# Optimization experiments

Measured on AMD Instinct MI355X. Metric: run time of the kernel, lower is better.

Reference implementation:

```python
import jax, jax.numpy as jnp
import numpy as np

N_NODES = 100000
N_EDGES = 2000000
D = 128
REL_TYPES = 64


def setup_inputs() -> dict:
    key = jax.random.key(0)
    k1, k2, k3, k4 = jax.random.split(key, 4)
    z = jax.random.normal(k1, (N_NODES, D), dtype=jnp.float32)
    edge_index = jax.random.randint(k2, (2, N_EDGES), 0, N_NODES, dtype=jnp.int64)
    rel_id = jax.random.randint(k3, (N_EDGES,), 0, REL_TYPES, dtype=jnp.int64)
    rel = jax.random.normal(k4, (REL_TYPES, D), dtype=jnp.float32)
    return {"z": z, "edge_index": edge_index, "rel_id": rel_id, "rel": rel}


def reference(z, edge_index, rel_id, rel):
    # DistMult: sigmoid(sum_d z[src,d] * rel[rel_id,d] * z[dst,d])
    src = z[edge_index[0]]          # [E, D]
    dst = z[edge_index[1]]          # [E, D]
    r = rel[rel_id]                 # [E, D]
    scores = jnp.sum(src * r * dst, axis=1)  # [E]
    return jax.nn.sigmoid(scores)
```

## Files before the change

kernel.cpp:

```cpp
#include <hip/hip_runtime.h>
#include <hip/hip_fp16.h>
#include <stdint.h>


#define NSRC 8
#define NDST 64
#define NBKT 512
#define CNT_STRIDE 16
#define SC_BLOCKS 512

__global__ __launch_bounds__(256) void convert_kernel(
    const float* __restrict__ x, __half* __restrict__ xh, int n8)
{
    const int i = blockIdx.x * blockDim.x + threadIdx.x;
    if (i >= n8) return;
    const float4 f0 = ((const float4*)x)[2 * i];
    const float4 f1 = ((const float4*)x)[2 * i + 1];
    union { __half2 h2[4]; uint4 u; } o;
    o.h2[0] = __floats2half2_rn(f0.x, f0.y);
    o.h2[1] = __floats2half2_rn(f0.z, f0.w);
    o.h2[2] = __floats2half2_rn(f1.x, f1.y);
    o.h2[3] = __floats2half2_rn(f1.z, f1.w);
    ((uint4*)xh)[i] = o.u;
}

__device__ __forceinline__ uint32_t bucket_of2(uint32_t s, uint32_t d, uint32_t nn) {
    uint32_t ss = (s * (uint32_t)NSRC) / nn; if (ss > NSRC - 1) ss = NSRC - 1;
    uint32_t ds = (d * (uint32_t)NDST) / nn; if (ds > NDST - 1) ds = NDST - 1;
    return ss * NDST + ds;
}

__global__ __launch_bounds__(256) void scatter_agg_kernel(
    const int* __restrict__ src, const int* __restrict__ dst,
    const int* __restrict__ relid, int E, int nn, int cap,
    uint32_t* __restrict__ counters, uint64_t* __restrict__ binned)
{
    __shared__ uint32_t hist[NBKT];
    __shared__ uint32_t cursor[NBKT];

    const int chunk = (E + (int)gridDim.x - 1) / (int)gridDim.x;
    const int lo = blockIdx.x * chunk;
    const int hi = (lo + chunk < E) ? lo + chunk : E;

    for (int t = threadIdx.x; t < NBKT; t += 256) hist[t] = 0;
    __syncthreads();

    for (int i = lo + (int)threadIdx.x; i < hi; i += 256) {
        const uint32_t b = bucket_of2((uint32_t)src[i], (uint32_t)dst[i], (uint32_t)nn);
        atomicAdd(&hist[b], 1u);
    }
    __syncthreads();

    for (int t = threadIdx.x; t < NBKT; t += 256) {
        const uint32_t c = hist[t];
        cursor[t] = c ? atomicAdd(&counters[t * CNT_STRIDE], c) : 0u;
    }
    __syncthreads();

    for (int i = lo + (int)threadIdx.x; i < hi; i += 256) {
        const uint32_t s = (uint32_t)src[i];
        const uint32_t d = (uint32_t)dst[i];
        const uint32_t r = (uint32_t)relid[i];
        const uint32_t b = bucket_of2(s, d, (uint32_t)nn);
        const uint32_t pos = atomicAdd(&cursor[b], 1u);
        if (pos < (uint32_t)cap)
            binned[(size_t)b * (size_t)cap + pos] =
                (uint64_t)s | ((uint64_t)d << 17) | ((uint64_t)r << 34) | ((uint64_t)i << 40);
    }
}

__global__ __launch_bounds__(256) void distmult_bucketed_kernel(
    const __half* __restrict__ zh,
    const uint64_t* __restrict__ binned,
    const uint32_t* __restrict__ counters,
    const __half* __restrict__ relh,
    float* __restrict__ out,
    int cap, int cpb)
{
    const int k     = blockIdx.x & 7;
    const int t     = blockIdx.x >> 3;
    const int j     = t / cpb;
    const int chunk = t - j * cpb;
    const int bkt   = k * NDST + j;

    uint32_t cnt = counters[bkt * CNT_STRIDE];
    if (cnt > (uint32_t)cap) cnt = (uint32_t)cap;
    const uint32_t el_blk = (uint32_t)chunk * 32u;
    if (el_blk >= cnt) return;

    __shared__ uint4 rel_lds[1024];
    {
        const uint4* rsrc = (const uint4*)relh;
        #pragma unroll
        for (int q = 0; q < 4; q++)
            rel_lds[threadIdx.x + 256 * q] = rsrc[threadIdx.x + 256 * q];
    }
    __syncthreads();

    const int g    = threadIdx.x >> 4;
    const int lane = threadIdx.x & 15;
    const uint32_t el0 = el_blk + (uint32_t)g * 2u;
    if (el0 >= cnt) return;
    const bool has1 = (el0 + 1u < cnt);

    const uint64_t* bb = binned + (size_t)bkt * (size_t)cap;
    const uint64_t p0 = bb[el0];
    const uint64_t p1 = has1 ? bb[el0 + 1u] : p0;

    const uint32_t s0 = (uint32_t)p0 & 0x1FFFFu;
    const uint32_t d0 = (uint32_t)(p0 >> 17) & 0x1FFFFu;
    const uint32_t r0 = (uint32_t)(p0 >> 34) & 0x3Fu;
    const uint32_t e0 = (uint32_t)(p0 >> 40);
    const uint32_t s1 = (uint32_t)p1 & 0x1FFFFu;
    const uint32_t d1 = (uint32_t)(p1 >> 17) & 0x1FFFFu;
    const uint32_t r1 = (uint32_t)(p1 >> 34) & 0x3Fu;
    const uint32_t e1 = (uint32_t)(p1 >> 40);

    union { uint4 u; __half2 h2[4]; } A0, B0, A1, B1, R0, R1;
    A0.u = ((const uint4*)(zh + (size_t)s0 * 128))[lane];
    B0.u = ((const uint4*)(zh + (size_t)d0 * 128))[lane];
    A1.u = ((const uint4*)(zh + (size_t)s1 * 128))[lane];
    B1.u = ((const uint4*)(zh + (size_t)d1 * 128))[lane];
    R0.u = rel_lds[r0 * 16 + lane];
    R1.u = rel_lds[r1 * 16 + lane];

    float v0 = 0.f, v1 = 0.f;
    #pragma unroll
    for (int q = 0; q < 4; q++) {
        const float2 a0 = __half22float2(A0.h2[q]);
        const float2 b0 = __half22float2(B0.h2[q]);
        const float2 c0 = __half22float2(R0.h2[q]);
        v0 += a0.x * c0.x * b0.x + a0.y * c0.y * b0.y;
        const float2 a1 = __half22float2(A1.h2[q]);
        const float2 b1 = __half22float2(B1.h2[q]);
        const float2 c1 = __half22float2(R1.h2[q]);
        v1 += a1.x * c1.x * b1.x + a1.y * c1.y * b1.y;
    }

    #pragma unroll
    for (int off = 8; off > 0; off >>= 1) {
        v0 += __shfl_down(v0, off, 16);
        v1 += __shfl_down(v1, off, 16);
    }

    if (lane == 0) {
        out[e0] = 1.0f / (1.0f + __expf(-v0));
        if (has1) out[e1] = 1.0f / (1.0f + __expf(-v1));
    }
}

__global__ __launch_bounds__(256) void distmult_f16_lds_kernel(
    const __half* __restrict__ zh,
    const int* __restrict__ src_idx, const int* __restrict__ dst_idx,
    const int* __restrict__ rel_id, const __half* __restrict__ relh,
    float* __restrict__ out, int E)
{
    __shared__ uint4 rel_lds[1024];
    {
        const uint4* rsrc = (const uint4*)relh;
        #pragma unroll
        for (int q = 0; q < 4; q++)
            rel_lds[threadIdx.x + 256 * q] = rsrc[threadIdx.x + 256 * q];
    }
    __syncthreads();

    const int gtid = blockIdx.x * blockDim.x + threadIdx.x;
    const int g = gtid >> 4;
    const int lane = threadIdx.x & 15;
    const int e0 = g * 2, e1 = e0 + 1;
    if (e0 >= E) return;
    const bool has1 = (e1 < E);

    const int s0 = src_idx[e0], d0 = dst_idx[e0], r0 = rel_id[e0];
    const int s1 = has1 ? src_idx[e1] : s0;
    const int d1 = has1 ? dst_idx[e1] : d0;
    const int r1 = has1 ? rel_id[e1]  : r0;

    union { uint4 u; __half2 h2[4]; } A0, B0, A1, B1, R0, R1;
    A0.u = ((const uint4*)(zh + (size_t)s0 * 128))[lane];
    B0.u = ((const uint4*)(zh + (size_t)d0 * 128))[lane];
    A1.u = ((const uint4*)(zh + (size_t)s1 * 128))[lane];
    B1.u = ((const uint4*)(zh + (size_t)d1 * 128))[lane];
    R0.u = rel_lds[r0 * 16 + lane];
    R1.u = rel_lds[r1 * 16 + lane];

    float v0 = 0.f, v1 = 0.f;
    #pragma unroll
    for (int q = 0; q < 4; q++) {
        const float2 a0 = __half22float2(A0.h2[q]);
        const float2 b0 = __half22float2(B0.h2[q]);
        const float2 c0 = __half22float2(R0.h2[q]);
        v0 += a0.x * c0.x * b0.x + a0.y * c0.y * b0.y;
        const float2 a1 = __half22float2(A1.h2[q]);
        const float2 b1 = __half22float2(B1.h2[q]);
        const float2 c1 = __half22float2(R1.h2[q]);
        v1 += a1.x * c1.x * b1.x + a1.y * c1.y * b1.y;
    }
    #pragma unroll
    for (int off = 8; off > 0; off >>= 1) {
        v0 += __shfl_down(v0, off, 16);
        v1 += __shfl_down(v1, off, 16);
    }
    if (lane == 0) {
        const float o0 = 1.0f / (1.0f + __expf(-v0));
        if (has1) {
            const float o1 = 1.0f / (1.0f + __expf(-v1));
            *((float2*)(out + e0)) = make_float2(o0, o1);
        } else {
            out[e0] = o0;
        }
    }
}

__global__ __launch_bounds__(256) void distmult_f32_kernel(
    const float* __restrict__ z,
    const int* __restrict__ src_idx, const int* __restrict__ dst_idx,
    const int* __restrict__ rel_id, const float* __restrict__ rel,
    float* __restrict__ out, int E)
{
    const int gtid = blockIdx.x * blockDim.x + threadIdx.x;
    const int e = gtid >> 4;
    const int lane = threadIdx.x & 15;
    if (e >= E) return;
    const int s = src_idx[e], d = dst_idx[e], r = rel_id[e];
    const float4* zs = (const float4*)(z + (size_t)s * 128);
    const float4* zd = (const float4*)(z + (size_t)d * 128);
    const float4* rr = (const float4*)(rel + (size_t)r * 128);
    const float4 a0 = zs[lane], a1 = zs[lane + 16];
    const float4 b0 = zd[lane], b1 = zd[lane + 16];
    const float4 c0 = rr[lane], c1 = rr[lane + 16];
    float v = a0.x * c0.x * b0.x + a0.y * c0.y * b0.y
            + a0.z * c0.z * b0.z + a0.w * c0.w * b0.w
            + a1.x * c1.x * b1.x + a1.y * c1.y * b1.y
            + a1.z * c1.z * b1.z + a1.w * c1.w * b1.w;
    #pragma unroll
    for (int off = 8; off > 0; off >>= 1) v += __shfl_down(v, off, 16);
    if (lane == 0) out[e] = 1.0f / (1.0f + __expf(-v));
}

extern "C" void kernel_launch(void* const* d_in, const int* in_sizes, int n_in,
                              void* d_out, int out_size, void* d_ws, size_t ws_size,
                              hipStream_t stream) {
    const float* z     = (const float*)d_in[0];
    const int*   eidx  = (const int*)d_in[1];
    const int*   relid = (const int*)d_in[2];
    const float* rel   = (const float*)d_in[3];
    float*       out   = (float*)d_out;

    const int nz   = in_sizes[0];
    const int E    = in_sizes[2];
    const int nrel = in_sizes[3];
    const int nn   = nz / 128;
    const int* src = eidx;
    const int* dst = eidx + E;

    const int mean_b = E / NBKT;
    int cap = mean_b + E / 8192 + 512;
    cap = (cap + 31) & ~31;
    const int cpb = cap / 32;

    const size_t sz_zh    = (size_t)nz * sizeof(__half);
    const size_t off_rh   = (sz_zh + 255) & ~(size_t)255;
    const size_t sz_rh    = (size_t)nrel * sizeof(__half);
    const size_t off_cnt  = (off_rh + sz_rh + 255) & ~(size_t)255;
    const size_t sz_cnt   = (size_t)NBKT * CNT_STRIDE * 4;
    const size_t off_bin  = (off_cnt + sz_cnt + 255) & ~(size_t)255;
    const size_t sz_bin   = (size_t)NBKT * (size_t)cap * 8;
    const size_t need     = off_bin + sz_bin;

    const bool rel_ok  = (nrel == 64 * 128);
    const bool bits_ok = (nn <= 131072) && (E <= (1 << 21)) && (nz % 8 == 0);

    if (ws_size >= need && rel_ok && bits_ok) {
        char* ws = (char*)d_ws;
        __half*   zh       = (__half*)(ws);
        __half*   rh       = (__half*)(ws + off_rh);
        uint32_t* counters = (uint32_t*)(ws + off_cnt);
        uint64_t* binned   = (uint64_t*)(ws + off_bin);

        const int n8z = nz / 8, n8r = nrel / 8;
        convert_kernel<<<(n8z + 255) / 256, 256, 0, stream>>>(z, zh, n8z);
        convert_kernel<<<(n8r + 255) / 256, 256, 0, stream>>>(rel, rh, n8r);
        hipMemsetAsync(counters, 0, sz_cnt, stream);
        scatter_agg_kernel<<<SC_BLOCKS, 256, 0, stream>>>(
            src, dst, relid, E, nn, cap, counters, binned);
        distmult_bucketed_kernel<<<NSRC * NDST * cpb, 256, 0, stream>>>(
            zh, binned, counters, rh, out, cap, cpb);
    } else if (ws_size >= off_rh + sz_rh && rel_ok && nz % 8 == 0) {
        __half* zh = (__half*)d_ws;
        __half* rh = (__half*)((char*)d_ws + off_rh);
        const int n8z = nz / 8, n8r = nrel / 8;
        convert_kernel<<<(n8z + 255) / 256, 256, 0, stream>>>(z, zh, n8z);
        convert_kernel<<<(n8r + 255) / 256, 256, 0, stream>>>(rel, rh, n8r);
        const int groups = (E + 1) / 2;
        const int blocks = (groups * 16 + 255) / 256;
        distmult_f16_lds_kernel<<<blocks, 256, 0, stream>>>(
            zh, src, dst, relid, rh, out, E);
    } else {
        const int blocks = (E * 16 + 255) / 256;
        distmult_f32_kernel<<<blocks, 256, 0, stream>>>(z, src, dst, relid, rel, out, E);
    }
}
```

Baseline: 265.1 us.

## Cache scatter payloads in registers, use 8-lane groups with fdot2

The scatter kernel now reads src, dst and rel_id once. It keeps each edge's packed payload and bucket in registers between the histogram pass and the write pass, where before it re-read the index arrays a second time. The bucketed scoring kernel now gives each edge to 8 lanes instead of two edges per 16 lanes. Each lane loads two 16-byte chunks, and the products are computed with packed half multiplies feeding the fdot2 builtin, which cuts conversion work and the shuffle depth. The risks are higher register pressure in scatter (16 payloads per thread), the chunk size now setting the grid size, and fp16 multiplication of a*r before accumulation, which lowers precision.

Result: faster. 231.2 us (-12.8%).

```diff
diff --git a/kernel.cpp b/kernel.cpp
--- a/kernel.cpp
+++ b/kernel.cpp
@@ -8,6 +8,35 @@
 #define NBKT 512
 #define CNT_STRIDE 16
 #define SC_BLOCKS 512
+#define PE 16
+
+#if defined(__has_builtin)
+#if __has_builtin(__builtin_amdgcn_fdot2)
+#define HAS_FDOT2 1
+#endif
+#endif
+
+typedef _Float16 hv2 __attribute__((ext_vector_type(2)));
+
+__device__ __forceinline__ float dot3_accum(uint32_t a, uint32_t r, uint32_t b,
+                                            float acc)
+{
+#ifdef HAS_FDOT2
+    union { uint32_t u; hv2 v; } A, R, B;
+    A.u = a; R.u = r; B.u = b;
+    const hv2 t = A.v * R.v;
+    return __builtin_amdgcn_fdot2(t, B.v, acc, false);
+#else
+    union { uint32_t u; __half2 h; } A, R, B;
+    A.u = a; R.u = r; B.u = b;
+    const float2 af = __half22float2(A.h);
+    const float2 rf = __half22float2(R.h);
+    const float2 bf = __half22float2(B.h);
+    acc = fmaf(af.x * rf.x, bf.x, acc);
+    acc = fmaf(af.y * rf.y, bf.y, acc);
+    return acc;
+#endif
+}
 
 __global__ __launch_bounds__(256) void convert_kernel(
     const float* __restrict__ x, __half* __restrict__ xh, int n8)
@@ -30,7 +59,7 @@
     return ss * NDST + ds;
 }
 
-__global__ __launch_bounds__(256) void scatter_agg_kernel(
+__global__ __launch_bounds__(256) void scatter_reg_kernel(
     const int* __restrict__ src, const int* __restrict__ dst,
     const int* __restrict__ relid, int E, int nn, int cap,
     uint32_t* __restrict__ counters, uint64_t* __restrict__ binned)
@@ -45,9 +74,24 @@
     for (int t = threadIdx.x; t < NBKT; t += 256) hist[t] = 0;
     __syncthreads();
 
-    for (int i = lo + (int)threadIdx.x; i < hi; i += 256) {
-        const uint32_t b = bucket_of2((uint32_t)src[i], (uint32_t)dst[i], (uint32_t)nn);
-        atomicAdd(&hist[b], 1u);
+    uint64_t pay[PE];
+    uint32_t bkt[PE];
+
+    #pragma unroll
+    for (int p = 0; p < PE; p++) {
+        const int i = lo + p * 256 + (int)threadIdx.x;
+        if (i < hi) {
+            const uint32_t s = (uint32_t)src[i];
+            const uint32_t d = (uint32_t)dst[i];
+            const uint32_t r = (uint32_t)relid[i];
+            const uint32_t b = bucket_of2(s, d, (uint32_t)nn);
+            pay[p] = (uint64_t)s | ((uint64_t)d << 17)
+                   | ((uint64_t)r << 34) | ((uint64_t)i << 40);
+            bkt[p] = b;
+            atomicAdd(&hist[b], 1u);
+        } else {
+            bkt[p] = 0xFFFFFFFFu;
+        }
     }
     __syncthreads();
 
@@ -57,19 +101,17 @@
     }
     __syncthreads();
 
-    for (int i = lo + (int)threadIdx.x; i < hi; i += 256) {
-        const uint32_t s = (uint32_t)src[i];
-        const uint32_t d = (uint32_t)dst[i];
-        const uint32_t r = (uint32_t)relid[i];
-        const uint32_t b = bucket_of2(s, d, (uint32_t)nn);
-        const uint32_t pos = atomicAdd(&cursor[b], 1u);
-        if (pos < (uint32_t)cap)
-            binned[(size_t)b * (size_t)cap + pos] =
-                (uint64_t)s | ((uint64_t)d << 17) | ((uint64_t)r << 34) | ((uint64_t)i << 40);
-    }
-}
-
-__global__ __launch_bounds__(256) void distmult_bucketed_kernel(
+    #pragma unroll
+    for (int p = 0; p < PE; p++) {
+        if (bkt[p] != 0xFFFFFFFFu) {
+            const uint32_t pos = atomicAdd(&cursor[bkt[p]], 1u);
+            if (pos < (uint32_t)cap)
+                binned[(size_t)bkt[p] * (size_t)cap + pos] = pay[p];
+        }
+    }
+}
+
+__global__ __launch_bounds__(256) void distmult_bucketed8_kernel(
     const __half* __restrict__ zh,
     const uint64_t* __restrict__ binned,
     const uint32_t* __restrict__ counters,
@@ -97,56 +139,41 @@
     }
     __syncthreads();
 
-    const int g    = threadIdx.x >> 4;
-    const int lane = threadIdx.x & 15;
-    const uint32_t el0 = el_blk + (uint32_t)g * 2u;
-    if (el0 >= cnt) return;
-    const bool has1 = (el0 + 1u < cnt);
-
-    const uint64_t* bb = binned + (size_t)bkt * (size_t)cap;
-    const uint64_t p0 = bb[el0];
-    const uint64_t p1 = has1 ? bb[el0 + 1u] : p0;
-
-    const uint32_t s0 = (uint32_t)p0 & 0x1FFFFu;
-    const uint32_t d0 = (uint32_t)(p0 >> 17) & 0x1FFFFu;
-    const uint32_t r0 = (uint32_t)(p0 >> 34) & 0x3Fu;
-    const uint32_t e0 = (uint32_t)(p0 >> 40);
-    const uint32_t s1 = (uint32_t)p1 & 0x1FFFFu;
-    const uint32_t d1 = (uint32_t)(p1 >> 17) & 0x1FFFFu;
-    const uint32_t r1 = (uint32_t)(p1 >> 34) & 0x3Fu;
-    const uint32_t e1 = (uint32_t)(p1 >> 40);
-
-    union { uint4 u; __half2 h2[4]; } A0, B0, A1, B1, R0, R1;
-    A0.u = ((const uint4*)(zh + (size_t)s0 * 128))[lane];
-    B0.u = ((const uint4*)(zh + (size_t)d0 * 128))[lane];
-    A1.u = ((const uint4*)(zh + (size_t)s1 * 128))[lane];
-    B1.u = ((const uint4*)(zh + (size_t)d1 * 128))[lane];
-    R0.u = rel_lds[r0 * 16 + lane];
-    R1.u = rel_lds[r1 * 16 + lane];
-
-    float v0 = 0.f, v1 = 0.f;
+    const int g    = threadIdx.x >> 3;
+    const int lane = threadIdx.x & 7;
+    const uint32_t el = el_blk + (uint32_t)g;
+    if (el >= cnt) return;
+
+    const uint64_t p = binned[(size_t)bkt * (size_t)cap + el];
+    const uint32_t s   = (uint32_t)p & 0x1FFFFu;
+    const uint32_t d   = (uint32_t)(p >> 17) & 0x1FFFFu;
+    const uint32_t r   = (uint32_t)(p >> 34) & 0x3Fu;
+    const uint32_t eid = (uint32_t)(p >> 40);
+
+    union U4 { uint4 q; uint32_t w[4]; };
+    const uint4* sb = (const uint4*)(zh + (size_t)s * 128);
+    const uint4* db = (const uint4*)(zh + (size_t)d * 128);
+    U4 A0, A1, B0, B1, R0, R1;
+    A0.q = sb[lane * 2];
+    A1.q = sb[lane * 2 + 1];
+    B0.q = db[lane * 2];
+    B1.q = db[lane * 2 + 1];
+    R0.q = rel_lds[r * 16 + lane * 2];
+    R1.q = rel_lds[r * 16 + lane * 2 + 1];
+
+    float acc = 0.f;
     #pragma unroll
     for (int q = 0; q < 4; q++) {
-        const float2 a0 = __half22float2(A0.h2[q]);
-        const float2 b0 = __half22float2(B0.h2[q]);
-        const float2 c0 = __half22float2(R0.h2[q]);
-        v0 += a0.x * c0.x * b0.x + a0.y * c0.y * b0.y;
-        const float2 a1 = __half22float2(A1.h2[q]);
-        const float2 b1 = __half22float2(B1.h2[q]);
-        const float2 c1 = __half22float2(R1.h2[q]);
-        v1 += a1.x * c1.x * b1.x + a1.y * c1.y * b1.y;
-    }
-
-    #pragma unroll
-    for (int off = 8; off > 0; off >>= 1) {
-        v0 += __shfl_down(v0, off, 16);
-        v1 += __shfl_down(v1, off, 16);
-    }
-
-    if (lane == 0) {
-        out[e0] = 1.0f / (1.0f + __expf(-v0));
-        if (has1) out[e1] = 1.0f / (1.0f + __expf(-v1));
-    }
+        acc = dot3_accum(A0.w[q], R0.w[q], B0.w[q], acc);
+        acc = dot3_accum(A1.w[q], R1.w[q], B1.w[q], acc);
+    }
+
+    #pragma unroll
+    for (int off = 4; off > 0; off >>= 1)
+        acc += __shfl_down(acc, off, 8);
+
+    if (lane == 0)
+        out[eid] = 1.0f / (1.0f + __expf(-acc));
 }
 
 __global__ __launch_bounds__(256) void distmult_f16_lds_kernel(
@@ -176,25 +203,20 @@
     const int d1 = has1 ? dst_idx[e1] : d0;
     const int r1 = has1 ? rel_id[e1]  : r0;
 
-    union { uint4 u; __half2 h2[4]; } A0, B0, A1, B1, R0, R1;
-    A0.u = ((const uint4*)(zh + (size_t)s0 * 128))[lane];
-    B0.u = ((const uint4*)(zh + (size_t)d0 * 128))[lane];
-    A1.u = ((const uint4*)(zh + (size_t)s1 * 128))[lane];
-    B1.u = ((const uint4*)(zh + (size_t)d1 * 128))[lane];
-    R0.u = rel_lds[r0 * 16 + lane];
-    R1.u = rel_lds[r1 * 16 + lane];
+    union U4 { uint4 q; uint32_t w[4]; };
+    U4 A0, B0, A1, B1, R0, R1;
+    A0.q = ((const uint4*)(zh + (size_t)s0 * 128))[lane];
+    B0.q = ((const uint4*)(zh + (size_t)d0 * 128))[lane];
+    A1.q = ((const uint4*)(zh + (size_t)s1 * 128))[lane];
+    B1.q = ((const uint4*)(zh + (size_t)d1 * 128))[lane];
+    R0.q = rel_lds[r0 * 16 + lane];
+    R1.q = rel_lds[r1 * 16 + lane];
 
     float v0 = 0.f, v1 = 0.f;
     #pragma unroll
     for (int q = 0; q < 4; q++) {
-        const float2 a0 = __half22float2(A0.h2[q]);
-        const float2 b0 = __half22float2(B0.h2[q]);
-        const float2 c0 = __half22float2(R0.h2[q]);
-        v0 += a0.x * c0.x * b0.x + a0.y * c0.y * b0.y;
-        const float2 a1 = __half22float2(A1.h2[q]);
-        const float2 b1 = __half22float2(B1.h2[q]);
-        const float2 c1 = __half22float2(R1.h2[q]);
-        v1 += a1.x * c1.x * b1.x + a1.y * c1.y * b1.y;
+        v0 = dot3_accum(A0.w[q], R0.w[q], B0.w[q], v0);
+        v1 = dot3_accum(A1.w[q], R1.w[q], B1.w[q], v1);
     }
     #pragma unroll
     for (int off = 8; off > 0; off >>= 1) {
@@ -259,6 +281,9 @@
     cap = (cap + 31) & ~31;
     const int cpb = cap / 32;
 
+    const int sc_blocks = ((E + PE * 256 - 1) / (PE * 256) > SC_BLOCKS)
+                        ? (E + PE * 256 - 1) / (PE * 256) : SC_BLOCKS;
+
     const size_t sz_zh    = (size_t)nz * sizeof(__half);
     const size_t off_rh   = (sz_zh + 255) & ~(size_t)255;
     const size_t sz_rh    = (size_t)nrel * sizeof(__half);
@@ -282,9 +307,9 @@
         convert_kernel<<<(n8z + 255) / 256, 256, 0, stream>>>(z, zh, n8z);
         convert_kernel<<<(n8r + 255) / 256, 256, 0, stream>>>(rel, rh, n8r);
         hipMemsetAsync(counters, 0, sz_cnt, stream);
-        scatter_agg_kernel<<<SC_BLOCKS, 256, 0, stream>>>(
+        scatter_reg_kernel<<<sc_blocks, 256, 0, stream>>>(
             src, dst, relid, E, nn, cap, counters, binned);
-        distmult_bucketed_kernel<<<NSRC * NDST * cpb, 256, 0, stream>>>(
+        distmult_bucketed8_kernel<<<NSRC * NDST * cpb, 256, 0, stream>>>(
             zh, binned, counters, rh, out, cap, cpb);
     } else if (ws_size >= off_rh + sz_rh && rel_ok && nz % 8 == 0) {
         __half* zh = (__half*)d_ws;
```
